# Performance work log

Measured on AMD Instinct MI355X. Metric: run time of the kernel, lower is better.

Reference implementation:

```python
import jax, jax.numpy as jnp
import numpy as np

B, T, F, E, H, D, L = 4096, 20, 32, 128, 2, 64, 3
EPS = 1e-5


def setup_inputs() -> dict:
    key = jax.random.key(0)
    ks = jax.random.split(key, 16)
    n = lambda k, s, sc=0.05: jax.random.normal(k, s, jnp.float32) * sc
    return {
        'tokens': jax.random.randint(ks[0], (B, T), 0, 50000),
        'field_ids': jax.random.randint(ks[1], (B, F - 1), 0, 1000),
        'word_emb': n(ks[2], (50000, 300)),
        'W_tok': n(ks[3], (300, E)),
        'field_tables': n(ks[4], (F - 1, 1000, E), E ** -0.5),
        'Wq': n(ks[5], (L, E, H * D)),
        'Wk': n(ks[6], (L, E, H * D)),
        'Wv': n(ks[7], (L, E, H * D)),
        'Wres': n(ks[8], (L, E, H * D)),
        'ln_g': jnp.ones((L, H * D), jnp.float32),
        'ln_b': jnp.zeros((L, H * D), jnp.float32),
        'dnn_W1': n(ks[9], (F * E, 1024)),
        'bn1_g': jnp.ones((1024,), jnp.float32), 'bn1_b': jnp.zeros((1024,), jnp.float32),
        'bn1_m': jnp.zeros((1024,), jnp.float32), 'bn1_v': jnp.ones((1024,), jnp.float32),
        'dnn_W2': n(ks[10], (1024, 512)),
        'bn2_g': jnp.ones((512,), jnp.float32), 'bn2_b': jnp.zeros((512,), jnp.float32),
        'bn2_m': jnp.zeros((512,), jnp.float32), 'bn2_v': jnp.ones((512,), jnp.float32),
        'dnn_W3': n(ks[11], (512, 128)),
        'dnn_b3': jnp.zeros((128,), jnp.float32),
        'W_last': n(ks[12], (F * H * D + 128, 1)),
        'b_last': jnp.zeros((1,), jnp.float32),
    }


def _layer_norm(o, g, b):
    mu = o.mean(-1, keepdims=True)
    var = o.var(-1, keepdims=True)
    return (o - mu) / jnp.sqrt(var + EPS) * g + b


def reference(tokens, field_ids, word_emb, W_tok, field_tables, Wq, Wk, Wv, Wres,
              ln_g, ln_b, dnn_W1, bn1_g, bn1_b, bn1_m, bn1_v, dnn_W2, bn2_g, bn2_b,
              bn2_m, bn2_v, dnn_W3, dnn_b3, W_last, b_last):
    # EmbeddingBag(mean) over tokens, then linear to emb_length
    tok_e = word_emb[tokens].mean(1) @ W_tok                      # [B, E]
    # per-field one-hot embedding lookup
    fld_e = field_tables[jnp.arange(F - 1)[None, :], field_ids]    # [B, F-1, E]
    emb = jnp.concatenate([tok_e[:, None, :], fld_e], 1)          # [B, F, E]

    x = emb
    for l in range(L):
        # split(num_out,-1)+cat(...,0) == reshape to heads
        q = (x @ Wq[l]).reshape(B, F, H, D)
        k = (x @ Wk[l]).reshape(B, F, H, D)
        v = (x @ Wv[l]).reshape(B, F, H, D)
        w = jax.nn.softmax(jnp.einsum('bqhd,bkhd->bhqk', q, k) / jnp.sqrt(jnp.float32(D)), -1)
        o = jnp.einsum('bhqk,bkhd->bqhd', w, v).reshape(B, F, H * D)
        o = jax.nn.relu(o + x @ Wres[l])
        x = _layer_norm(o, ln_g[l], ln_b[l])

    att = x.reshape(B, F * H * D)

    # DNN branch (eval mode: BN uses running stats, dropout off)
    h = emb.reshape(B, F * E)
    h = jax.nn.relu((h @ dnn_W1 - bn1_m) / jnp.sqrt(bn1_v + EPS) * bn1_g + bn1_b)
    h = jax.nn.relu((h @ dnn_W2 - bn2_m) / jnp.sqrt(bn2_v + EPS) * bn2_g + bn2_b)
    h = h @ dnn_W3 + dnn_b3

    out = jnp.concatenate([att, h], 1) @ W_last + b_last          # [B, 1]
    return jax.nn.sigmoid(out)
```

## Files before the change

### kernel.cpp

```cpp
#include <hip/hip_runtime.h>
#include <hip/hip_bf16.h>
#include <cstdint>

#define B_  4096
#define T_  20
#define F_  32
#define E_  128
#define H_  2
#define D_  64
#define L_  3
#define HD_ 128
#define EPS_ 1e-5f

typedef __bf16 bfv8 __attribute__((ext_vector_type(8)));
typedef __bf16 bfv4 __attribute__((ext_vector_type(4)));
typedef float  f32x4 __attribute__((ext_vector_type(4)));

__device__ __forceinline__ f32x4 mfma16(bfv8 a, bfv8 b, f32x4 c) {
    return __builtin_amdgcn_mfma_f32_16x16x32_bf16(a, b, c, 0, 0, 0);
}

__device__ __forceinline__ void gload16(const __bf16* g, __bf16* l) {
    __builtin_amdgcn_global_load_lds(
        (const __attribute__((address_space(1))) void*)(g),
        (__attribute__((address_space(3))) void*)(l),
        16, 0, 0);
}

__global__ __launch_bounds__(256) void pack_weights_kernel(
    const float* __restrict__ Wq, const float* __restrict__ Wk,
    const float* __restrict__ Wv, const float* __restrict__ Wres,
    __bf16* __restrict__ out)
{
    int mi = blockIdx.x;
    int tile = blockIdx.y;
    int l = mi >> 2, p = mi & 3;
    const float* Wb = (p == 0 ? Wq : p == 1 ? Wk : p == 2 ? Wv : Wres) + l * 16384;
    int tid = threadIdx.x;
    int ks = tid >> 6, lane = tid & 63;
    int l15 = lane & 15, lgg = lane >> 4;
    const float* src = Wb + (ks * 32 + lgg * 8) * HD_ + tile * 16 + l15;
    __bf16* dst = out + (int64_t)mi * 16384 + ((tile * 4 + ks) * 64 + lane) * 8;
    #pragma unroll
    for (int t = 0; t < 8; t++) dst[t] = (__bf16)src[t * HD_];
}

__global__ __launch_bounds__(256) void transpose_pack_kernel(
    const float* __restrict__ in, __bf16* __restrict__ out, int K, int N)
{
    __shared__ float t[64][65];
    int k0 = blockIdx.x * 64, n0 = blockIdx.y * 64;
    int r = threadIdx.x >> 4, c = (threadIdx.x & 15) * 4;
    for (int rr = r; rr < 64; rr += 16) {
        float4 v = *(const float4*)&in[(int64_t)(k0 + rr) * N + n0 + c];
        t[rr][c] = v.x; t[rr][c + 1] = v.y; t[rr][c + 2] = v.z; t[rr][c + 3] = v.w;
    }
    __syncthreads();
    for (int rr = r; rr < 64; rr += 16) {
        bfv4 o;
        o[0] = (__bf16)t[c + 0][rr];
        o[1] = (__bf16)t[c + 1][rr];
        o[2] = (__bf16)t[c + 2][rr];
        o[3] = (__bf16)t[c + 3][rr];
        *(bfv4*)&out[(int64_t)(n0 + rr) * K + k0 + c] = o;
    }
}

__global__ __launch_bounds__(128) void tok_embed_kernel(
    const int* __restrict__ tokens, const float* __restrict__ word_emb,
    const float* __restrict__ W_tok, __bf16* __restrict__ embbf)
{
    int b = blockIdx.x;
    int tid = threadIdx.x;
    __shared__ float m[300];
    float a0 = 0.f, a1 = 0.f, a2 = 0.f;
    const int* tb = tokens + b * T_;
    for (int t = 0; t < T_; t++) {
        const float* row = word_emb + (int64_t)tb[t] * 300;
        a0 += row[tid];
        a1 += row[tid + 128];
        if (tid < 44) a2 += row[tid + 256];
    }
    m[tid]       = a0 * (1.f / T_);
    m[tid + 128] = a1 * (1.f / T_);
    if (tid < 44) m[tid + 256] = a2 * (1.f / T_);
    __syncthreads();
    float s = 0.f;
    for (int e = 0; e < 300; e++) s = fmaf(m[e], W_tok[e * E_ + tid], s);
    embbf[(int64_t)b * (F_ * E_) + tid] = (__bf16)s;
}

__global__ __launch_bounds__(256) void field_gather_kernel(
    const int* __restrict__ field_ids, const float* __restrict__ field_tables,
    __bf16* __restrict__ embbf)
{
    int64_t idx = (int64_t)blockIdx.x * blockDim.x + threadIdx.x;
    if (idx >= (int64_t)B_ * 31 * 32) return;
    int c = (int)(idx & 31);
    int64_t tmp = idx >> 5;
    int f = (int)(tmp % 31);
    int b = (int)(tmp / 31);
    int id = field_ids[b * 31 + f];
    const float4* src = (const float4*)field_tables;
    float4 val = src[(int64_t)(f * 1000 + id) * 32 + c];
    bfv4 o;
    o[0] = (__bf16)val.x; o[1] = (__bf16)val.y;
    o[2] = (__bf16)val.z; o[3] = (__bf16)val.w;
    *(bfv4*)&embbf[(int64_t)b * 4096 + (1 + f) * 128 + c * 4] = o;
}

template <int OUTBF, int EPI>
__global__ __launch_bounds__(256) void gemm_bt_bf16(
    const __bf16* __restrict__ A, const __bf16* __restrict__ Bt,
    void* __restrict__ Cout, int M, int N, int K,
    const float* __restrict__ gp, const float* __restrict__ bp,
    const float* __restrict__ mp, const float* __restrict__ vp)
{
    __shared__ __bf16 As[128 * 64];
    __shared__ __bf16 Bs[64 * 64];
    const int tid = threadIdx.x;
    const int wid = tid >> 6, lane = tid & 63;
    const int l15 = lane & 15, lg = lane >> 4;
    const int wr = wid >> 1, wc = wid & 1;
    const int bm = blockIdx.x, bn = blockIdx.y;

    const int srow = lane >> 3, sp = lane & 7;
    const __bf16* Ag[4]; const __bf16* Bg[2];
    __bf16* Ad[4]; __bf16* Bd[2];
    #pragma unroll
    for (int ga = 0; ga < 4; ga++) {
        int row = wid * 32 + ga * 8 + srow;
        int slot = sp ^ (row & 7);
        Ag[ga] = A + (int64_t)(bm * 128 + row) * K + slot * 8;
        Ad[ga] = &As[(wid * 32 + ga * 8) * 64];
    }
    #pragma unroll
    for (int gb = 0; gb < 2; gb++) {
        int row = wid * 16 + gb * 8 + srow;
        int slot = sp ^ (row & 7);
        Bg[gb] = Bt + (int64_t)(bn * 64 + row) * K + slot * 8;
        Bd[gb] = &Bs[(wid * 16 + gb * 8) * 64];
    }

    int ar[2][4], br2[2][2];
    #pragma unroll
    for (int ks = 0; ks < 2; ks++) {
        #pragma unroll
        for (int mi = 0; mi < 4; mi++) {
            int row = wr * 64 + mi * 16 + l15;
            ar[ks][mi] = row * 64 + (((ks * 4 + lg) ^ (row & 7)) * 8);
        }
        #pragma unroll
        for (int ni = 0; ni < 2; ni++) {
            int row = wc * 32 + ni * 16 + l15;
            br2[ks][ni] = row * 64 + (((ks * 4 + lg) ^ (row & 7)) * 8);
        }
    }

    f32x4 acc[4][2];
    #pragma unroll
    for (int mi = 0; mi < 4; mi++)
        #pragma unroll
        for (int ni = 0; ni < 2; ni++) acc[mi][ni] = (f32x4){0.f, 0.f, 0.f, 0.f};

    for (int k0 = 0; k0 < K; k0 += 64) {
        #pragma unroll
        for (int ga = 0; ga < 4; ga++) gload16(Ag[ga] + k0, Ad[ga]);
        #pragma unroll
        for (int gb = 0; gb < 2; gb++) gload16(Bg[gb] + k0, Bd[gb]);
        __syncthreads();
        #pragma unroll
        for (int ks = 0; ks < 2; ks++) {
            bfv8 af[4], bf2[2];
            #pragma unroll
            for (int mi = 0; mi < 4; mi++) af[mi] = *(const bfv8*)&As[ar[ks][mi]];
            #pragma unroll
            for (int ni = 0; ni < 2; ni++) bf2[ni] = *(const bfv8*)&Bs[br2[ks][ni]];
            #pragma unroll
            for (int mi = 0; mi < 4; mi++)
                #pragma unroll
                for (int ni = 0; ni < 2; ni++)
                    acc[mi][ni] = mfma16(af[mi], bf2[ni], acc[mi][ni]);
        }
        __syncthreads();
    }

    float inv[2], sh[2];
    #pragma unroll
    for (int ni = 0; ni < 2; ni++) {
        int col = bn * 64 + wc * 32 + ni * 16 + l15;
        if constexpr (EPI == 0) {
            float iv = rsqrtf(vp[col] + EPS_) * gp[col];
            inv[ni] = iv;
            sh[ni] = bp[col] - mp[col] * iv;
        } else {
            inv[ni] = 1.f;
            sh[ni] = bp[col];
        }
    }
    #pragma unroll
    for (int mi = 0; mi < 4; mi++)
        #pragma unroll
        for (int ni = 0; ni < 2; ni++) {
            int col = bn * 64 + wc * 32 + ni * 16 + l15;
            #pragma unroll
            for (int r = 0; r < 4; r++) {
                int row = bm * 128 + wr * 64 + mi * 16 + lg * 4 + r;
                float y = fmaf(acc[mi][ni][r], inv[ni], sh[ni]);
                if constexpr (EPI == 0) y = fmaxf(y, 0.f);
                if constexpr (OUTBF)
                    ((__bf16*)Cout)[(int64_t)row * N + col] = (__bf16)y;
                else
                    ((float*)Cout)[(int64_t)row * N + col] = y;
            }
        }
}

__global__ __launch_bounds__(512, 4) void attn3_head_kernel(
    const __bf16* __restrict__ embbf, const __bf16* __restrict__ pkw,
    const float* __restrict__ lng, const float* __restrict__ lnb,
    const float* __restrict__ h3, const float* __restrict__ Wl,
    const float* __restrict__ bl, float* __restrict__ out)
{
    __shared__ __bf16 smem[8192 * 4 + 4096];
    __shared__ float  part[2][128];
    __bf16* xs  = smem;
    __bf16* qf  = smem + 8192;
    __bf16* kf  = smem + 16384;
    __bf16* vtf = smem + 24576;
    __bf16* pf  = smem + 32768;
    __bf16* wrs = qf;

    const int tid = threadIdx.x;
    const int wid = tid >> 6, lane = tid & 63;
    const int l15 = lane & 15, lg = lane >> 4;
    const int arow = wid >> 2, h = (wid >> 1) & 1, qh = wid & 1;
    const int q = qh * 16 + l15;
    const int half = (lg & 1) * 4;

    {
        const __bf16* src = embbf + (int64_t)blockIdx.x * 8192;
        #pragma unroll
        for (int u = 0; u < 2; u++) {
            int g = u * 512 + tid;
            int ln = g & 63;
            int fld = (((g >> 8) & 1) << 4) + (ln & 15);
            int e0 = ((g >> 6) & 3) * 32 + (ln >> 4) * 8;
            int br = g >> 9;
            bfv8 v = *(const bfv8*)&src[br * 4096 + fld * 128 + e0];
            *(bfv8*)&xs[g * 8] = v;
        }
    }
    __syncthreads();

    float head_partial = 0.f;

    for (int l = 0; l < L_; l++) {
        #pragma unroll 1
        for (int cc = 0; cc < 3; cc++) {
            const int col = wid * 3 + cc;
            const int mat = col >> 3, m = col & 7;
            const __bf16* W = pkw + (l * 4 + mat) * 16384;
            bfv8 wf[4];
            #pragma unroll
            for (int ks = 0; ks < 4; ks++)
                wf[ks] = *(const bfv8*)(W + ((m * 4 + ks) * 64 + lane) * 8);
            f32x4 pc[4];
            #pragma unroll
            for (int i = 0; i < 4; i++) pc[i] = (f32x4){0.f, 0.f, 0.f, 0.f};

            if (mat == 2) {
                #pragma unroll
                for (int i = 0; i < 4; i++) {
                    int gbase = ((i >> 1) * 8 + (i & 1) * 4) * 64;
                    #pragma unroll
                    for (int ks = 0; ks < 4; ks++) {
                        bfv8 xv = *(const bfv8*)&xs[(gbase + ks * 64 + lane) * 8];
                        pc[i] = mfma16(xv, wf[ks], pc[i]);
                    }
                }
            } else {
                #pragma unroll
                for (int i = 0; i < 4; i++) {
                    int gbase = ((i >> 1) * 8 + (i & 1) * 4) * 64;
                    #pragma unroll
                    for (int ks = 0; ks < 4; ks++) {
                        bfv8 xv = *(const bfv8*)&xs[(gbase + ks * 64 + lane) * 8];
                        pc[i] = mfma16(wf[ks], xv, pc[i]);
                    }
                }
            }

            if (mat == 0) {
                const int ln2 = ((((m << 1) + (lg >> 1)) & 3) << 4) + l15;
                #pragma unroll
                for (int i = 0; i < 4; i++) {
                    bfv4 v4;
                    #pragma unroll
                    for (int r = 0; r < 4; r++) v4[r] = (__bf16)(pc[i][r] * 0.125f);
                    int g = ((i >> 1) * 8 + (i & 1) * 4 + (m >> 1)) * 64 + ln2;
                    *(bfv4*)&qf[g * 8 + half] = v4;
                }
            } else if (mat == 1) {
                const int ln2 = ((((m << 1) + (lg >> 1)) & 3) << 4) + l15;
                #pragma unroll
                for (int i = 0; i < 4; i++) {
                    bfv4 v4;
                    #pragma unroll
                    for (int r = 0; r < 4; r++) v4[r] = (__bf16)pc[i][r];
                    int g = ((i >> 1) * 8 + (i & 1) * 4 + (m >> 1)) * 64 + ln2;
                    *(bfv4*)&kf[g * 8 + half] = v4;
                }
            } else {
                #pragma unroll
                for (int i = 0; i < 4; i++) {
                    bfv4 v4;
                    #pragma unroll
                    for (int r = 0; r < 4; r++) v4[r] = (__bf16)pc[i][r];
                    int lnv = ((((i & 1) * 2 + (lg >> 1)) & 3) << 4) + l15;
                    int g = ((i >> 1) * 8 + m) * 64 + lnv;
                    *(bfv4*)&vtf[g * 8 + half] = v4;
                }
            }
        }
        __syncthreads();

        f32x4 sc2[2] = {(f32x4){0.f, 0.f, 0.f, 0.f}, (f32x4){0.f, 0.f, 0.f, 0.f}};
        #pragma unroll
        for (int ksp = 0; ksp < 2; ksp++) {
            int dks = h * 2 + ksp;
            bfv8 qb = *(const bfv8*)&qf[((arow * 8 + qh * 4 + dks) * 64 + lane) * 8];
            #pragma unroll
            for (int km = 0; km < 2; km++) {
                bfv8 kb = *(const bfv8*)&kf[((arow * 8 + km * 4 + dks) * 64 + lane) * 8];
                sc2[km] = mfma16(kb, qb, sc2[km]);
            }
        }
        __syncthreads();

        {
            const __bf16* Wr = pkw + (l * 4 + 3) * 16384;
            #pragma unroll
            for (int c = 0; c < 4; c++) {
                int g = c * 512 + tid;
                gload16(Wr + g * 8, wrs + g * 8);
            }
        }
        float mx = -1e30f;
        #pragma unroll
        for (int km = 0; km < 2; km++)
            #pragma unroll
            for (int r = 0; r < 4; r++) mx = fmaxf(mx, sc2[km][r]);
        mx = fmaxf(mx, __shfl_xor(mx, 16));
        mx = fmaxf(mx, __shfl_xor(mx, 32));
        float pv[2][4];
        float sum = 0.f;
        #pragma unroll
        for (int km = 0; km < 2; km++)
            #pragma unroll
            for (int r = 0; r < 4; r++) {
                float e = __expf(sc2[km][r] - mx);
                pv[km][r] = e; sum += e;
            }
        sum += __shfl_xor(sum, 16);
        sum += __shfl_xor(sum, 32);
        float inv = 1.f / sum;

        __bf16* pw = pf + wid * 512;
        #pragma unroll
        for (int km = 0; km < 2; km++) {
            int ln2 = (((km * 2 + (lg >> 1)) & 3) << 4) + l15;
            bfv4 v4;
            #pragma unroll
            for (int r = 0; r < 4; r++) v4[r] = (__bf16)(pv[km][r] * inv);
            *(bfv4*)&pw[ln2 * 8 + half] = v4;
        }
        bfv8 pb = *(const bfv8*)&pw[lane * 8];
        f32x4 o[4];
        #pragma unroll
        for (int dm = 0; dm < 4; dm++) {
            bfv8 va = *(const bfv8*)&vtf[((arow * 8 + h * 4 + dm) * 64 + lane) * 8];
            o[dm] = mfma16(va, pb, (f32x4){0.f, 0.f, 0.f, 0.f});
        }
        __syncthreads();

        f32x4 macc[4];
        {
            bfv8 xr[4];
            #pragma unroll
            for (int ks = 0; ks < 4; ks++)
                xr[ks] = *(const bfv8*)&xs[((arow * 8 + qh * 4 + ks) * 64 + lane) * 8];
            #pragma unroll
            for (int dm = 0; dm < 4; dm++) {
                macc[dm] = (f32x4){0.f, 0.f, 0.f, 0.f};
                int m = h * 4 + dm;
                #pragma unroll
                for (int ks = 0; ks < 4; ks++) {
                    bfv8 wf = *(const bfv8*)&wrs[((m * 4 + ks) * 64 + lane) * 8];
                    macc[dm] = mfma16(wf, xr[ks], macc[dm]);
                }
            }
        }

        float yv[4][4];
        float s1 = 0.f, s2 = 0.f;
        #pragma unroll
        for (int dm = 0; dm < 4; dm++) {
            #pragma unroll
            for (int r = 0; r < 4; r++) {
                float v = fmaxf(o[dm][r] + macc[dm][r], 0.f);
                yv[dm][r] = v;
                s1 += v; s2 += v * v;
            }
        }
        s1 += __shfl_xor(s1, 16); s1 += __shfl_xor(s1, 32);
        s2 += __shfl_xor(s2, 16); s2 += __shfl_xor(s2, 32);
        if (lg == 0) { part[arow][q * 4 + h * 2] = s1; part[arow][q * 4 + h * 2 + 1] = s2; }
        __syncthreads();

        f32x4 pt = *(const f32x4*)&part[arow][q * 4];
        float mean = (pt[0] + pt[2]) * (1.f / 128.f);
        float var  = (pt[1] + pt[3]) * (1.f / 128.f) - mean * mean;
        float rstd = rsqrtf(var + EPS_);
        const float* lgp = lng + l * HD_;
        const float* lbp = lnb + l * HD_;

        if (l < L_ - 1) {
            #pragma unroll
            for (int dm = 0; dm < 4; dm++) {
                int j = h * 64 + dm * 16 + lg * 4;
                float4 g  = *(const float4*)(lgp + j);
                float4 bb = *(const float4*)(lbp + j);
                bfv4 y;
                y[0] = (__bf16)((yv[dm][0] - mean) * rstd * g.x + bb.x);
                y[1] = (__bf16)((yv[dm][1] - mean) * rstd * g.y + bb.y);
                y[2] = (__bf16)((yv[dm][2] - mean) * rstd * g.z + bb.z);
                y[3] = (__bf16)((yv[dm][3] - mean) * rstd * g.w + bb.w);
                int ks2 = h * 2 + (dm >> 1);
                int ln2 = (((dm * 2 + (lg >> 1)) & 3) << 4) + l15;
                int g2 = (arow * 8 + qh * 4 + ks2) * 64 + ln2;
                *(bfv4*)&xs[g2 * 8 + half] = y;
            }
            __syncthreads();
        } else {
            #pragma unroll
            for (int dm = 0; dm < 4; dm++) {
                int j = h * 64 + dm * 16 + lg * 4;
                float4 g  = *(const float4*)(lgp + j);
                float4 bb = *(const float4*)(lbp + j);
                float4 w  = *(const float4*)(Wl + q * HD_ + j);
                head_partial = fmaf((yv[dm][0] - mean) * rstd * g.x + bb.x, w.x, head_partial);
                head_partial = fmaf((yv[dm][1] - mean) * rstd * g.y + bb.y, w.y, head_partial);
                head_partial = fmaf((yv[dm][2] - mean) * rstd * g.z + bb.z, w.z, head_partial);
                head_partial = fmaf((yv[dm][3] - mean) * rstd * g.w + bb.w, w.w, head_partial);
            }
        }
    }

    float* red = (float*)pf;
    red[tid] = head_partial;
    __syncthreads();
    if ((wid & 3) == 0) {
        int br = wid >> 2;
        int base = br * 256;
        float s = red[base + lane] + red[base + 64 + lane]
                + red[base + 128 + lane] + red[base + 192 + lane];
        int64_t b0 = (int64_t)blockIdx.x * 2 + br;
        s += h3[b0 * 128 + lane]      * Wl[4096 + lane];
        s += h3[b0 * 128 + 64 + lane] * Wl[4096 + 64 + lane];
        #pragma unroll
        for (int off = 32; off; off >>= 1) s += __shfl_down(s, off);
        if (lane == 0) out[b0] = 1.f / (1.f + __expf(-(s + bl[0])));
    }
}

extern "C" void kernel_launch(void* const* d_in, const int* in_sizes, int n_in,
                              void* d_out, int out_size, void* d_ws, size_t ws_size,
                              hipStream_t stream)
{
    const int*   tokens       = (const int*)  d_in[0];
    const int*   field_ids    = (const int*)  d_in[1];
    const float* word_emb     = (const float*)d_in[2];
    const float* W_tok        = (const float*)d_in[3];
    const float* field_tables = (const float*)d_in[4];
    const float* Wq           = (const float*)d_in[5];
    const float* Wk           = (const float*)d_in[6];
    const float* Wv           = (const float*)d_in[7];
    const float* Wres         = (const float*)d_in[8];
    const float* ln_g         = (const float*)d_in[9];
    const float* ln_b         = (const float*)d_in[10];
    const float* dnn_W1       = (const float*)d_in[11];
    const float* bn1_g        = (const float*)d_in[12];
    const float* bn1_b        = (const float*)d_in[13];
    const float* bn1_m        = (const float*)d_in[14];
    const float* bn1_v        = (const float*)d_in[15];
    const float* dnn_W2       = (const float*)d_in[16];
    const float* bn2_g        = (const float*)d_in[17];
    const float* bn2_b        = (const float*)d_in[18];
    const float* bn2_m        = (const float*)d_in[19];
    const float* bn2_v        = (const float*)d_in[20];
    const float* dnn_W3       = (const float*)d_in[21];
    const float* dnn_b3       = (const float*)d_in[22];
    const float* W_last       = (const float*)d_in[23];
    const float* b_last       = (const float*)d_in[24];
    float* out = (float*)d_out;

    const int64_t embN = (int64_t)B_ * F_ * E_;
    __bf16* embbf = (__bf16*)d_ws;
    float*  h3    = (float*)(embbf + embN);
    __bf16* pkw   = (__bf16*)(h3 + (int64_t)B_ * 128);
    __bf16* W1t   = pkw + 12 * 16384;
    __bf16* W2t   = W1t + (int64_t)1024 * 4096;
    __bf16* W3t   = W2t + (int64_t)512 * 1024;
    __bf16* h1bf  = W3t + (int64_t)128 * 512;
    __bf16* h2bf  = h1bf + (int64_t)B_ * 1024;

    pack_weights_kernel<<<dim3(12, 8), 256, 0, stream>>>(Wq, Wk, Wv, Wres, pkw);
    transpose_pack_kernel<<<dim3(64, 16), 256, 0, stream>>>(dnn_W1, W1t, 4096, 1024);
    transpose_pack_kernel<<<dim3(16, 8), 256, 0, stream>>>(dnn_W2, W2t, 1024, 512);
    transpose_pack_kernel<<<dim3(8, 2), 256, 0, stream>>>(dnn_W3, W3t, 512, 128);

    tok_embed_kernel<<<B_, 128, 0, stream>>>(tokens, word_emb, W_tok, embbf);
    field_gather_kernel<<<(B_ * 31 * 32) / 256, 256, 0, stream>>>(field_ids, field_tables, embbf);

    gemm_bt_bf16<1, 0><<<dim3(32, 16), 256, 0, stream>>>(
        embbf, W1t, h1bf, B_, 1024, 4096, bn1_g, bn1_b, bn1_m, bn1_v);
    gemm_bt_bf16<1, 0><<<dim3(32, 8), 256, 0, stream>>>(
        h1bf, W2t, h2bf, B_, 512, 1024, bn2_g, bn2_b, bn2_m, bn2_v);
    gemm_bt_bf16<0, 1><<<dim3(32, 2), 256, 0, stream>>>(
        h2bf, W3t, h3, B_, 128, 512, nullptr, dnn_b3, nullptr, nullptr);

    attn3_head_kernel<<<B_ / 2, 512, 0, stream>>>(
        embbf, pkw, ln_g, ln_b, h3, W_last, b_last, out);
}
```

Measured before the change: 237.7 us.

## Merge pack and embedding launches, use 128x128 tile GEMM for first DNN layer

Folds the four weight-packing kernels into one launch and the token-embedding and field-gather kernels into one launch to cut launch overhead and idle gaps. Adds a 128x128-tile MFMA GEMM with fused BatchNorm+ReLU for the large first DNN layer, doubling B-tile reuse and halving the grid. The larger tile raises register and LDS use, which may lower occupancy, and the new GEMM has no double buffering.

```diff
diff --git a/kernel.cpp b/kernel.cpp
--- a/kernel.cpp
+++ b/kernel.cpp
@@ -27,29 +27,12 @@
         16, 0, 0);
 }
 
-__global__ __launch_bounds__(256) void pack_weights_kernel(
-    const float* __restrict__ Wq, const float* __restrict__ Wk,
-    const float* __restrict__ Wv, const float* __restrict__ Wres,
-    __bf16* __restrict__ out)
-{
-    int mi = blockIdx.x;
-    int tile = blockIdx.y;
-    int l = mi >> 2, p = mi & 3;
-    const float* Wb = (p == 0 ? Wq : p == 1 ? Wk : p == 2 ? Wv : Wres) + l * 16384;
-    int tid = threadIdx.x;
-    int ks = tid >> 6, lane = tid & 63;
-    int l15 = lane & 15, lgg = lane >> 4;
-    const float* src = Wb + (ks * 32 + lgg * 8) * HD_ + tile * 16 + l15;
-    __bf16* dst = out + (int64_t)mi * 16384 + ((tile * 4 + ks) * 64 + lane) * 8;
-    #pragma unroll
-    for (int t = 0; t < 8; t++) dst[t] = (__bf16)src[t * HD_];
-}
-
-__global__ __launch_bounds__(256) void transpose_pack_kernel(
-    const float* __restrict__ in, __bf16* __restrict__ out, int K, int N)
+__device__ void transpose_pack_body(const float* __restrict__ in,
+                                    __bf16* __restrict__ out,
+                                    int K, int N, int bx, int by)
 {
     __shared__ float t[64][65];
-    int k0 = blockIdx.x * 64, n0 = blockIdx.y * 64;
+    int k0 = bx * 64, n0 = by * 64;
     int r = threadIdx.x >> 4, c = (threadIdx.x & 15) * 4;
     for (int rr = r; rr < 64; rr += 16) {
         float4 v = *(const float4*)&in[(int64_t)(k0 + rr) * N + n0 + c];
@@ -66,47 +49,170 @@
     }
 }
 
-__global__ __launch_bounds__(128) void tok_embed_kernel(
+__global__ __launch_bounds__(256) void pack_all_kernel(
+    const float* __restrict__ Wq, const float* __restrict__ Wk,
+    const float* __restrict__ Wv, const float* __restrict__ Wres,
+    __bf16* __restrict__ pkw,
+    const float* __restrict__ dW1, __bf16* __restrict__ W1t,
+    const float* __restrict__ dW2, __bf16* __restrict__ W2t,
+    const float* __restrict__ dW3, __bf16* __restrict__ W3t)
+{
+    int id = blockIdx.x;
+    if (id < 96) {
+        int mi = id >> 3, tile = id & 7;
+        int l = mi >> 2, p = mi & 3;
+        const float* Wb = (p == 0 ? Wq : p == 1 ? Wk : p == 2 ? Wv : Wres) + l * 16384;
+        int tid = threadIdx.x;
+        int ks = tid >> 6, lane = tid & 63;
+        int l15 = lane & 15, lgg = lane >> 4;
+        const float* src = Wb + (ks * 32 + lgg * 8) * HD_ + tile * 16 + l15;
+        __bf16* dst = pkw + (int64_t)mi * 16384 + ((tile * 4 + ks) * 64 + lane) * 8;
+        #pragma unroll
+        for (int t = 0; t < 8; t++) dst[t] = (__bf16)src[t * HD_];
+    } else if (id < 1120) {
+        int t = id - 96;
+        transpose_pack_body(dW1, W1t, 4096, 1024, t & 63, t >> 6);
+    } else if (id < 1248) {
+        int t = id - 1120;
+        transpose_pack_body(dW2, W2t, 1024, 512, t & 15, t >> 4);
+    } else {
+        int t = id - 1248;
+        transpose_pack_body(dW3, W3t, 512, 128, t & 7, t >> 3);
+    }
+}
+
+__global__ __launch_bounds__(256) void embed2_kernel(
     const int* __restrict__ tokens, const float* __restrict__ word_emb,
-    const float* __restrict__ W_tok, __bf16* __restrict__ embbf)
-{
-    int b = blockIdx.x;
-    int tid = threadIdx.x;
-    __shared__ float m[300];
-    float a0 = 0.f, a1 = 0.f, a2 = 0.f;
-    const int* tb = tokens + b * T_;
-    for (int t = 0; t < T_; t++) {
-        const float* row = word_emb + (int64_t)tb[t] * 300;
-        a0 += row[tid];
-        a1 += row[tid + 128];
-        if (tid < 44) a2 += row[tid + 256];
-    }
-    m[tid]       = a0 * (1.f / T_);
-    m[tid + 128] = a1 * (1.f / T_);
-    if (tid < 44) m[tid + 256] = a2 * (1.f / T_);
-    __syncthreads();
-    float s = 0.f;
-    for (int e = 0; e < 300; e++) s = fmaf(m[e], W_tok[e * E_ + tid], s);
-    embbf[(int64_t)b * (F_ * E_) + tid] = (__bf16)s;
-}
-
-__global__ __launch_bounds__(256) void field_gather_kernel(
+    const float* __restrict__ W_tok,
     const int* __restrict__ field_ids, const float* __restrict__ field_tables,
     __bf16* __restrict__ embbf)
 {
-    int64_t idx = (int64_t)blockIdx.x * blockDim.x + threadIdx.x;
-    if (idx >= (int64_t)B_ * 31 * 32) return;
-    int c = (int)(idx & 31);
-    int64_t tmp = idx >> 5;
-    int f = (int)(tmp % 31);
-    int b = (int)(tmp / 31);
-    int id = field_ids[b * 31 + f];
-    const float4* src = (const float4*)field_tables;
-    float4 val = src[(int64_t)(f * 1000 + id) * 32 + c];
-    bfv4 o;
-    o[0] = (__bf16)val.x; o[1] = (__bf16)val.y;
-    o[2] = (__bf16)val.z; o[3] = (__bf16)val.w;
-    *(bfv4*)&embbf[(int64_t)b * 4096 + (1 + f) * 128 + c * 4] = o;
+    if (blockIdx.x < 2048) {
+        __shared__ float m[2][304];
+        int half = threadIdx.x >> 7, t7 = threadIdx.x & 127;
+        int b = blockIdx.x * 2 + half;
+        float a0 = 0.f, a1 = 0.f, a2 = 0.f;
+        const int* tb = tokens + b * T_;
+        for (int t = 0; t < T_; t++) {
+            const float* row = word_emb + (int64_t)tb[t] * 300;
+            a0 += row[t7];
+            a1 += row[t7 + 128];
+            if (t7 < 44) a2 += row[t7 + 256];
+        }
+        m[half][t7]       = a0 * (1.f / T_);
+        m[half][t7 + 128] = a1 * (1.f / T_);
+        if (t7 < 44) m[half][t7 + 256] = a2 * (1.f / T_);
+        __syncthreads();
+        float s = 0.f;
+        for (int e = 0; e < 300; e++) s = fmaf(m[half][e], W_tok[e * E_ + t7], s);
+        embbf[(int64_t)b * (F_ * E_) + t7] = (__bf16)s;
+    } else {
+        int64_t base = (int64_t)(blockIdx.x - 2048) * 1024 + threadIdx.x;
+        #pragma unroll
+        for (int u = 0; u < 4; u++) {
+            int64_t idx = base + u * 256;
+            int c = (int)(idx & 31);
+            int64_t tmp = idx >> 5;
+            int f = (int)(tmp % 31);
+            int b = (int)(tmp / 31);
+            int ident = field_ids[b * 31 + f];
+            const float4* src = (const float4*)field_tables;
+            float4 val = src[(int64_t)(f * 1000 + ident) * 32 + c];
+            bfv4 o;
+            o[0] = (__bf16)val.x; o[1] = (__bf16)val.y;
+            o[2] = (__bf16)val.z; o[3] = (__bf16)val.w;
+            *(bfv4*)&embbf[(int64_t)b * 4096 + (1 + f) * 128 + c * 4] = o;
+        }
+    }
+}
+
+__global__ __launch_bounds__(256) void gemm128_bt_bf16_bn(
+    const __bf16* __restrict__ A, const __bf16* __restrict__ Bt,
+    __bf16* __restrict__ C, int M, int N, int K,
+    const float* __restrict__ gp, const float* __restrict__ bp,
+    const float* __restrict__ mp, const float* __restrict__ vp)
+{
+    __shared__ __bf16 As[128 * 64];
+    __shared__ __bf16 Bs[128 * 64];
+    const int tid = threadIdx.x;
+    const int wid = tid >> 6, lane = tid & 63;
+    const int l15 = lane & 15, lg = lane >> 4;
+    const int wr = wid >> 1, wc = wid & 1;
+    const int bm = blockIdx.x, bn = blockIdx.y;
+
+    const int srow = lane >> 3, sp = lane & 7;
+    const __bf16* Ag[4]; const __bf16* Bg[4];
+    __bf16* Ad[4]; __bf16* Bd[4];
+    #pragma unroll
+    for (int ga = 0; ga < 4; ga++) {
+        int row = wid * 32 + ga * 8 + srow;
+        int slot = sp ^ (row & 7);
+        Ag[ga] = A  + (int64_t)(bm * 128 + row) * K + slot * 8;
+        Bg[ga] = Bt + (int64_t)(bn * 128 + row) * K + slot * 8;
+        Ad[ga] = &As[(wid * 32 + ga * 8) * 64];
+        Bd[ga] = &Bs[(wid * 32 + ga * 8) * 64];
+    }
+
+    int ar[2][4], br[2][4];
+    #pragma unroll
+    for (int ks = 0; ks < 2; ks++) {
+        #pragma unroll
+        for (int mi = 0; mi < 4; mi++) {
+            int rowa = wr * 64 + mi * 16 + l15;
+            ar[ks][mi] = rowa * 64 + (((ks * 4 + lg) ^ (rowa & 7)) * 8);
+            int rowb = wc * 64 + mi * 16 + l15;
+            br[ks][mi] = rowb * 64 + (((ks * 4 + lg) ^ (rowb & 7)) * 8);
+        }
+    }
+
+    f32x4 acc[4][4];
+    #pragma unroll
+    for (int mi = 0; mi < 4; mi++)
+        #pragma unroll
+        for (int ni = 0; ni < 4; ni++) acc[mi][ni] = (f32x4){0.f, 0.f, 0.f, 0.f};
+
+    for (int k0 = 0; k0 < K; k0 += 64) {
+        #pragma unroll
+        for (int ga = 0; ga < 4; ga++) gload16(Ag[ga] + k0, Ad[ga]);
+        #pragma unroll
+        for (int ga = 0; ga < 4; ga++) gload16(Bg[ga] + k0, Bd[ga]);
+        __syncthreads();
+        #pragma unroll
+        for (int ks = 0; ks < 2; ks++) {
+            bfv8 af[4], bf[4];
+            #pragma unroll
+            for (int mi = 0; mi < 4; mi++) af[mi] = *(const bfv8*)&As[ar[ks][mi]];
+            #pragma unroll
+            for (int ni = 0; ni < 4; ni++) bf[ni] = *(const bfv8*)&Bs[br[ks][ni]];
+            #pragma unroll
+            for (int mi = 0; mi < 4; mi++)
+                #pragma unroll
+                for (int ni = 0; ni < 4; ni++)
+                    acc[mi][ni] = mfma16(af[mi], bf[ni], acc[mi][ni]);
+        }
+        __syncthreads();
+    }
+
+    float inv[4], sh[4];
+    #pragma unroll
+    for (int ni = 0; ni < 4; ni++) {
+        int col = bn * 128 + wc * 64 + ni * 16 + l15;
+        float iv = rsqrtf(vp[col] + EPS_) * gp[col];
+        inv[ni] = iv;
+        sh[ni] = bp[col] - mp[col] * iv;
+    }
+    #pragma unroll
+    for (int mi = 0; mi < 4; mi++)
+        #pragma unroll
+        for (int ni = 0; ni < 4; ni++) {
+            int col = bn * 128 + wc * 64 + ni * 16 + l15;
+            #pragma unroll
+            for (int r = 0; r < 4; r++) {
+                int row = bm * 128 + wr * 64 + mi * 16 + lg * 4 + r;
+                float y = fmaxf(fmaf(acc[mi][ni][r], inv[ni], sh[ni]), 0.f);
+                C[(int64_t)row * N + col] = (__bf16)y;
+            }
+        }
 }
 
 template <int OUTBF, int EPI>
@@ -515,15 +621,13 @@
     __bf16* h1bf  = W3t + (int64_t)128 * 512;
     __bf16* h2bf  = h1bf + (int64_t)B_ * 1024;
 
-    pack_weights_kernel<<<dim3(12, 8), 256, 0, stream>>>(Wq, Wk, Wv, Wres, pkw);
-    transpose_pack_kernel<<<dim3(64, 16), 256, 0, stream>>>(dnn_W1, W1t, 4096, 1024);
-    transpose_pack_kernel<<<dim3(16, 8), 256, 0, stream>>>(dnn_W2, W2t, 1024, 512);
-    transpose_pack_kernel<<<dim3(8, 2), 256, 0, stream>>>(dnn_W3, W3t, 512, 128);
-
-    tok_embed_kernel<<<B_, 128, 0, stream>>>(tokens, word_emb, W_tok, embbf);
-    field_gather_kernel<<<(B_ * 31 * 32) / 256, 256, 0, stream>>>(field_ids, field_tables, embbf);
-
-    gemm_bt_bf16<1, 0><<<dim3(32, 16), 256, 0, stream>>>(
+    pack_all_kernel<<<1264, 256, 0, stream>>>(
+        Wq, Wk, Wv, Wres, pkw, dnn_W1, W1t, dnn_W2, W2t, dnn_W3, W3t);
+
+    embed2_kernel<<<6016, 256, 0, stream>>>(
+        tokens, word_emb, W_tok, field_ids, field_tables, embbf);
+
+    gemm128_bt_bf16_bn<<<dim3(32, 8), 256, 0, stream>>>(
         embbf, W1t, h1bf, B_, 1024, 4096, bn1_g, bn1_b, bn1_m, bn1_v);
     gemm_bt_bf16<1, 0><<<dim3(32, 8), 256, 0, stream>>>(
         h1bf, W2t, h2bf, B_, 512, 1024, bn2_g, bn2_b, bn2_m, bn2_v);
```

Result: no change. 237.9 us (+0.1%).
